# Optimization experiments

Hardware: AMD Instinct MI355X
Metric: run time of the kernel (lower is better)

Reference implementation:

```python
import jax, jax.numpy as jnp
import numpy as np

HIDDEN = 1024
HEADS = 12
HEAD_DIM = 64
NEG = -1e12


def _rope(x):
    # x: [B, N, H, d], rotate along seq axis (axis 1), interleaved pairs
    B, N, H, d = x.shape
    inv_freq = 1.0 / (10000.0 ** (jnp.arange(0, d, 2, dtype=jnp.float32) / d))  # [d/2]
    pos = jnp.arange(N, dtype=jnp.float32)
    ang = pos[:, None] * inv_freq[None, :]                 # [N, d/2]
    sin = jnp.repeat(jnp.sin(ang), 2, axis=-1)[None, :, None, :]  # [1,N,1,d]
    cos = jnp.repeat(jnp.cos(ang), 2, axis=-1)[None, :, None, :]
    even = x[..., ::2]
    odd = x[..., 1::2]
    rot = jnp.stack([-odd, even], axis=-1).reshape(B, N, H, d)
    return x * cos + rot * sin


def setup_inputs() -> dict:
    key = jax.random.key(0)
    k1, k2, k3, k4 = jax.random.split(key, 4)
    hidden_states = jax.random.normal(k1, (16, 512, HIDDEN), dtype=jnp.float32)
    attention_weights = jax.random.randint(k2, (16, 512), 0, 2, dtype=jnp.int32)
    W = jax.random.normal(k3, (HIDDEN, HEADS * HEAD_DIM * 2), dtype=jnp.float32) * 0.02
    b = jax.random.normal(k4, (HEADS * HEAD_DIM * 2,), dtype=jnp.float32) * 0.02
    return {"hidden_states": hidden_states, "attention_weights": attention_weights, "W": W, "b": b}


def reference(hidden_states, attention_weights, W, b):
    B, N, _ = hidden_states.shape
    proj = hidden_states @ W + b                            # [B,N,H*2*d]
    proj = proj.reshape(B, N, HEADS, 2, HEAD_DIM)
    q, k = proj[..., 0, :], proj[..., 1, :]                 # [B,N,H,d]
    q = _rope(q)
    k = _rope(k)
    q = q / (HEAD_DIM ** 0.5)
    scores = jnp.einsum('bnhd,bmhd->bhnm', q, k)            # [B,H,N,N]
    # mask padded keys (key dim only, matching the torch repeat pattern)
    key_mask = (attention_weights == 0)[:, None, None, :]   # [B,1,1,N]
    scores = jnp.where(key_mask, NEG, scores)
    # mask diagonal
    diag = jnp.eye(N, dtype=bool)[None, None, :, :]
    scores = jnp.where(diag, NEG, scores)
    return jax.nn.sigmoid(scores)
```

## Files before the change

### kernel.cpp

```cpp
#include <hip/hip_runtime.h>

#define HEADS 12
#define HIDDEN 1024
#define NOUT 1536
#define SEQ 512

typedef __bf16 bf16x8 __attribute__((ext_vector_type(8)));
typedef float f32x4 __attribute__((ext_vector_type(4)));

__device__ __forceinline__ void gload_lds16(const void* g, void* l) {
  __builtin_amdgcn_global_load_lds(
      (const __attribute__((address_space(1))) unsigned int*)g,
      (__attribute__((address_space(3))) unsigned int*)l, 16, 0, 0);
}

__device__ __forceinline__ unsigned short f2bf(float f) {
  union { float f; unsigned u; } x;
  x.f = f;
  unsigned r = x.u + 0x7fffu + ((x.u >> 16) & 1u);
  return (unsigned short)(r >> 16);
}

__global__ __launch_bounds__(256) void k_convert_hidden(const float* __restrict__ in,
                                                        unsigned short* __restrict__ out) {
  int i = blockIdx.x * 256 + threadIdx.x;
  float4 v = ((const float4*)in)[i];
  ushort4 o;
  o.x = f2bf(v.x); o.y = f2bf(v.y); o.z = f2bf(v.z); o.w = f2bf(v.w);
  ((ushort4*)out)[i] = o;
}

__global__ __launch_bounds__(256) void k_transpose_w(const float* __restrict__ W,
                                                     unsigned short* __restrict__ Wt) {
  __shared__ unsigned short t[32][33];
  int n0 = blockIdx.x * 32;
  int k0 = blockIdx.y * 32;
  int tx = threadIdx.x & 31;
  int ty = threadIdx.x >> 5;
#pragma unroll
  for (int i = 0; i < 4; ++i) {
    int k = k0 + ty + i * 8;
    t[ty + i * 8][tx] = f2bf(W[(size_t)k * NOUT + n0 + tx]);
  }
  __syncthreads();
#pragma unroll
  for (int i = 0; i < 4; ++i) {
    int n = n0 + ty + i * 8;
    Wt[(size_t)n * HIDDEN + k0 + tx] = t[tx][ty + i * 8];
  }
}

__global__ __launch_bounds__(256) void k_trig(float2* __restrict__ trig) {
  int i = blockIdx.x * 256 + threadIdx.x;
  int pos = i >> 5, j = i & 31;
  float inv = 1.0f / powf(10000.0f, (float)(2 * j) * (1.0f / 64.0f));
  float ang = (float)pos * inv;
  trig[i] = make_float2(cosf(ang), sinf(ang));
}

__global__ __launch_bounds__(256) void k_proj(const unsigned short* __restrict__ A,
                                              const unsigned short* __restrict__ Bt,
                                              const float* __restrict__ bias,
                                              const float2* __restrict__ trig,
                                              unsigned short* __restrict__ qb,
                                              unsigned short* __restrict__ kb) {
  __shared__ unsigned short As[128 * 64];
  __shared__ unsigned short Bs[128 * 64];
  const int h = blockIdx.x;
  const int m0 = blockIdx.y * 128;
  const int n0 = h * 128;
  const int tid = threadIdx.x;
  const int wave = tid >> 6, lane = tid & 63;
  const int l15 = lane & 15, l4 = lane >> 4;
  const int wr = wave >> 1, wc = wave & 1;

  f32x4 acc[4][4];
#pragma unroll
  for (int a = 0; a < 4; ++a)
#pragma unroll
    for (int b2 = 0; b2 < 4; ++b2) acc[a][b2] = (f32x4){0.f, 0.f, 0.f, 0.f};

  for (int kt = 0; kt < 16; ++kt) {
    __syncthreads();
    const int kbase = kt * 64;
#pragma unroll
    for (int i = 0; i < 4; ++i) {
      int chunk = i * 256 + tid;
      int r = chunk >> 3, c8 = chunk & 7;
      gload_lds16(A + (size_t)(m0 + r) * HIDDEN + kbase + c8 * 8, As + chunk * 8);
      gload_lds16(Bt + (size_t)(n0 + r) * HIDDEN + kbase + c8 * 8, Bs + chunk * 8);
    }
    asm volatile("s_waitcnt vmcnt(0)" ::: "memory");
    __syncthreads();
#pragma unroll
    for (int kk = 0; kk < 2; ++kk) {
      bf16x8 af[4], bv[4];
#pragma unroll
      for (int mi = 0; mi < 4; ++mi)
        af[mi] = *(const bf16x8*)(As + (wr * 64 + mi * 16 + l15) * 64 + kk * 32 + l4 * 8);
#pragma unroll
      for (int ni = 0; ni < 4; ++ni)
        bv[ni] = *(const bf16x8*)(Bs + (wc * 64 + ni * 16 + l15) * 64 + kk * 32 + l4 * 8);
#pragma unroll
      for (int mi = 0; mi < 4; ++mi)
#pragma unroll
        for (int ni = 0; ni < 4; ++ni)
          acc[mi][ni] = __builtin_amdgcn_mfma_f32_16x16x32_bf16(af[mi], bv[ni], acc[mi][ni], 0, 0, 0);
    }
  }

#pragma unroll
  for (int ni = 0; ni < 4; ++ni) {
    const int c = wc * 64 + ni * 16 + l15;
    const int qk = c >> 6;
    const int d = c & 63;
    const int j = d >> 1;
    const int odd = d & 1;
    const float bias_v = bias[n0 + c];
    unsigned short* dst = qk ? kb : qb;
    const float scale = qk ? 1.0f : 0.125f;
#pragma unroll
    for (int mi = 0; mi < 4; ++mi) {
#pragma unroll
      for (int jj = 0; jj < 4; ++jj) {
        const int row = wr * 64 + mi * 16 + l4 * 4 + jj;
        const int m = m0 + row;
        const int bb = m >> 9, pos = m & 511;
        float v = acc[mi][ni][jj] + bias_v;
        float p = __shfl_xor(v, 1);
        float2 cs = trig[pos * 32 + j];
        float o = odd ? (v * cs.x + p * cs.y) : (v * cs.x - p * cs.y);
        o *= scale;
        dst[(((size_t)bb * HEADS + h) * SEQ + pos) * 64 + d] = f2bf(o);
      }
    }
  }
}

__global__ __launch_bounds__(256) void k_scores(const unsigned short* __restrict__ qb,
                                                const unsigned short* __restrict__ kb,
                                                const int* __restrict__ aw,
                                                float* __restrict__ out) {
  __shared__ unsigned short Qs[128 * 64];
  __shared__ unsigned short Ks[128 * 64];
  const int bh = blockIdx.y;
  const int b = bh / HEADS;
  const int tq = blockIdx.x & 3, tk = blockIdx.x >> 2;
  const int q0 = tq * 128, k0 = tk * 128;
  const int tid = threadIdx.x;
  const int wave = tid >> 6, lane = tid & 63;
  const int l15 = lane & 15, l4 = lane >> 4;
  const int wr = wave >> 1, wc = wave & 1;

  const unsigned short* qsrc = qb + (size_t)bh * SEQ * 64;
  const unsigned short* ksrc = kb + (size_t)bh * SEQ * 64;

#pragma unroll
  for (int i = 0; i < 4; ++i) {
    int chunk = i * 256 + tid;
    int r = chunk >> 3, c8 = chunk & 7;
    gload_lds16(qsrc + (size_t)(q0 + r) * 64 + c8 * 8, Qs + chunk * 8);
    gload_lds16(ksrc + (size_t)(k0 + r) * 64 + c8 * 8, Ks + chunk * 8);
  }

  f32x4 acc[4][4];
#pragma unroll
  for (int a = 0; a < 4; ++a)
#pragma unroll
    for (int b2 = 0; b2 < 4; ++b2) acc[a][b2] = (f32x4){0.f, 0.f, 0.f, 0.f};

  asm volatile("s_waitcnt vmcnt(0)" ::: "memory");
  __syncthreads();

#pragma unroll
  for (int kk = 0; kk < 2; ++kk) {
    bf16x8 qf[4], kf[4];
#pragma unroll
    for (int mi = 0; mi < 4; ++mi)
      qf[mi] = *(const bf16x8*)(Qs + (wr * 64 + mi * 16 + l15) * 64 + kk * 32 + l4 * 8);
#pragma unroll
    for (int ni = 0; ni < 4; ++ni)
      kf[ni] = *(const bf16x8*)(Ks + (wc * 64 + ni * 16 + l15) * 64 + kk * 32 + l4 * 8);
#pragma unroll
    for (int mi = 0; mi < 4; ++mi)
#pragma unroll
      for (int ni = 0; ni < 4; ++ni)
        acc[mi][ni] = __builtin_amdgcn_mfma_f32_16x16x32_bf16(qf[mi], kf[ni], acc[mi][ni], 0, 0, 0);
  }

#pragma unroll
  for (int ni = 0; ni < 4; ++ni) {
    const int c = wc * 64 + ni * 16 + l15;
    const int key = k0 + c;
    const int awv = aw[b * SEQ + key];
#pragma unroll
    for (int mi = 0; mi < 4; ++mi) {
#pragma unroll
      for (int jj = 0; jj < 4; ++jj) {
        const int row = wr * 64 + mi * 16 + l4 * 4 + jj;
        const int nq = q0 + row;
        float s = acc[mi][ni][jj];
        float o = (awv == 0 || nq == key) ? 0.0f : 1.0f / (1.0f + __expf(-s));
        out[((size_t)bh * SEQ + nq) * SEQ + key] = o;
      }
    }
  }
}

extern "C" void kernel_launch(void* const* d_in, const int* in_sizes, int n_in,
                              void* d_out, int out_size, void* d_ws, size_t ws_size,
                              hipStream_t stream) {
  const float* hidden = (const float*)d_in[0];
  const int* aw = (const int*)d_in[1];
  const float* W = (const float*)d_in[2];
  const float* bias = (const float*)d_in[3];
  float* out = (float*)d_out;

  char* ws = (char*)d_ws;
  unsigned short* hidA = (unsigned short*)ws;
  unsigned short* Wt = (unsigned short*)(ws + 16777216);
  unsigned short* qb = (unsigned short*)(ws + 19922944);
  unsigned short* kb = (unsigned short*)(ws + 32505856);
  float2* trig = (float2*)(ws + 45088768);

  k_convert_hidden<<<8192, 256, 0, stream>>>(hidden, hidA);
  k_transpose_w<<<dim3(48, 32), 256, 0, stream>>>(W, Wt);
  k_trig<<<64, 256, 0, stream>>>(trig);
  k_proj<<<dim3(12, 64), 256, 0, stream>>>(hidA, Wt, bias, trig, qb, kb);
  k_scores<<<dim3(16, 192), 256, 0, stream>>>(qb, kb, aw, out);
}
```

Before: 131.0 us.

## Fuse prep kernels, swizzle block order for XCDs, loop key tiles in scores

Merges the hidden convert, weight transpose and trig table kernels into one launch, which removes two kernel launch gaps. It also remaps block indices with a stride-8 swizzle so neighbouring tiles land on the same XCD. The scores kernel now keeps one Q tile in LDS and loops over all four key tiles, reloading only K. This cuts the number of scores blocks from 3072 to 768, which reduces parallelism, and each K reload is serialized with barriers and no overlap.

```diff
diff --git a/kernel.cpp b/kernel.cpp
--- a/kernel.cpp
+++ b/kernel.cpp
@@ -21,41 +21,48 @@
   return (unsigned short)(r >> 16);
 }
 
-__global__ __launch_bounds__(256) void k_convert_hidden(const float* __restrict__ in,
-                                                        unsigned short* __restrict__ out) {
-  int i = blockIdx.x * 256 + threadIdx.x;
-  float4 v = ((const float4*)in)[i];
-  ushort4 o;
-  o.x = f2bf(v.x); o.y = f2bf(v.y); o.z = f2bf(v.z); o.w = f2bf(v.w);
-  ((ushort4*)out)[i] = o;
-}
-
-__global__ __launch_bounds__(256) void k_transpose_w(const float* __restrict__ W,
-                                                     unsigned short* __restrict__ Wt) {
+__device__ __forceinline__ int swz8(int b, int per) {
+  return (b & 7) * per + (b >> 3);
+}
+
+__global__ __launch_bounds__(256) void k_prep(const float* __restrict__ hidden,
+                                              unsigned short* __restrict__ hidA,
+                                              const float* __restrict__ W,
+                                              unsigned short* __restrict__ Wt,
+                                              float2* __restrict__ trig) {
   __shared__ unsigned short t[32][33];
-  int n0 = blockIdx.x * 32;
-  int k0 = blockIdx.y * 32;
-  int tx = threadIdx.x & 31;
-  int ty = threadIdx.x >> 5;
-#pragma unroll
-  for (int i = 0; i < 4; ++i) {
-    int k = k0 + ty + i * 8;
-    t[ty + i * 8][tx] = f2bf(W[(size_t)k * NOUT + n0 + tx]);
-  }
-  __syncthreads();
-#pragma unroll
-  for (int i = 0; i < 4; ++i) {
-    int n = n0 + ty + i * 8;
-    Wt[(size_t)n * HIDDEN + k0 + tx] = t[tx][ty + i * 8];
-  }
-}
-
-__global__ __launch_bounds__(256) void k_trig(float2* __restrict__ trig) {
-  int i = blockIdx.x * 256 + threadIdx.x;
-  int pos = i >> 5, j = i & 31;
-  float inv = 1.0f / powf(10000.0f, (float)(2 * j) * (1.0f / 64.0f));
-  float ang = (float)pos * inv;
-  trig[i] = make_float2(cosf(ang), sinf(ang));
+  const int bid = blockIdx.x;
+  const int tid = threadIdx.x;
+  if (bid < 8192) {
+    int i = bid * 256 + tid;
+    float4 v = ((const float4*)hidden)[i];
+    ushort4 o;
+    o.x = f2bf(v.x); o.y = f2bf(v.y); o.z = f2bf(v.z); o.w = f2bf(v.w);
+    ((ushort4*)hidA)[i] = o;
+  } else if (bid < 8192 + 1536) {
+    int tt = bid - 8192;
+    int n0 = (tt % 48) * 32;
+    int k0 = (tt / 48) * 32;
+    int tx = tid & 31;
+    int ty = tid >> 5;
+#pragma unroll
+    for (int i = 0; i < 4; ++i) {
+      int k = k0 + ty + i * 8;
+      t[ty + i * 8][tx] = f2bf(W[(size_t)k * NOUT + n0 + tx]);
+    }
+    __syncthreads();
+#pragma unroll
+    for (int i = 0; i < 4; ++i) {
+      int n = n0 + ty + i * 8;
+      Wt[(size_t)n * HIDDEN + k0 + tx] = t[tx][ty + i * 8];
+    }
+  } else {
+    int i = (bid - 9728) * 256 + tid;
+    int pos = i >> 5, j = i & 31;
+    float inv = 1.0f / powf(10000.0f, (float)(2 * j) * (1.0f / 64.0f));
+    float ang = (float)pos * inv;
+    trig[i] = make_float2(cosf(ang), sinf(ang));
+  }
 }
 
 __global__ __launch_bounds__(256) void k_proj(const unsigned short* __restrict__ A,
@@ -66,8 +73,9 @@
                                               unsigned short* __restrict__ kb) {
   __shared__ unsigned short As[128 * 64];
   __shared__ unsigned short Bs[128 * 64];
-  const int h = blockIdx.x;
-  const int m0 = blockIdx.y * 128;
+  const int lin = swz8(blockIdx.x, 96);
+  const int h = lin % 12;
+  const int m0 = (lin / 12) * 128;
   const int n0 = h * 128;
   const int tid = threadIdx.x;
   const int wave = tid >> 6, lane = tid & 63;
@@ -143,66 +151,80 @@
                                                 float* __restrict__ out) {
   __shared__ unsigned short Qs[128 * 64];
   __shared__ unsigned short Ks[128 * 64];
-  const int bh = blockIdx.y;
+  const int lin = swz8(blockIdx.x, 96);
+  const int bh = lin >> 2;
   const int b = bh / HEADS;
-  const int tq = blockIdx.x & 3, tk = blockIdx.x >> 2;
-  const int q0 = tq * 128, k0 = tk * 128;
+  const int q0 = (lin & 3) * 128;
   const int tid = threadIdx.x;
   const int wave = tid >> 6, lane = tid & 63;
   const int l15 = lane & 15, l4 = lane >> 4;
   const int wr = wave >> 1, wc = wave & 1;
 
-  const unsigned short* qsrc = qb + (size_t)bh * SEQ * 64;
+  const unsigned short* qsrc = qb + (size_t)bh * SEQ * 64 + (size_t)q0 * 64;
   const unsigned short* ksrc = kb + (size_t)bh * SEQ * 64;
 
 #pragma unroll
   for (int i = 0; i < 4; ++i) {
     int chunk = i * 256 + tid;
     int r = chunk >> 3, c8 = chunk & 7;
-    gload_lds16(qsrc + (size_t)(q0 + r) * 64 + c8 * 8, Qs + chunk * 8);
-    gload_lds16(ksrc + (size_t)(k0 + r) * 64 + c8 * 8, Ks + chunk * 8);
-  }
-
-  f32x4 acc[4][4];
-#pragma unroll
-  for (int a = 0; a < 4; ++a)
-#pragma unroll
-    for (int b2 = 0; b2 < 4; ++b2) acc[a][b2] = (f32x4){0.f, 0.f, 0.f, 0.f};
-
+    gload_lds16(qsrc + (size_t)r * 64 + c8 * 8, Qs + chunk * 8);
+    gload_lds16(ksrc + (size_t)r * 64 + c8 * 8, Ks + chunk * 8);
+  }
   asm volatile("s_waitcnt vmcnt(0)" ::: "memory");
   __syncthreads();
 
-#pragma unroll
-  for (int kk = 0; kk < 2; ++kk) {
-    bf16x8 qf[4], kf[4];
-#pragma unroll
-    for (int mi = 0; mi < 4; ++mi)
-      qf[mi] = *(const bf16x8*)(Qs + (wr * 64 + mi * 16 + l15) * 64 + kk * 32 + l4 * 8);
-#pragma unroll
-    for (int ni = 0; ni < 4; ++ni)
-      kf[ni] = *(const bf16x8*)(Ks + (wc * 64 + ni * 16 + l15) * 64 + kk * 32 + l4 * 8);
-#pragma unroll
-    for (int mi = 0; mi < 4; ++mi)
+  for (int tk = 0; tk < 4; ++tk) {
+    const int k0 = tk * 128;
+    f32x4 acc[4][4];
+#pragma unroll
+    for (int a = 0; a < 4; ++a)
+#pragma unroll
+      for (int b2 = 0; b2 < 4; ++b2) acc[a][b2] = (f32x4){0.f, 0.f, 0.f, 0.f};
+
+#pragma unroll
+    for (int kk = 0; kk < 2; ++kk) {
+      bf16x8 qf[4], kf[4];
+#pragma unroll
+      for (int mi = 0; mi < 4; ++mi)
+        qf[mi] = *(const bf16x8*)(Qs + (wr * 64 + mi * 16 + l15) * 64 + kk * 32 + l4 * 8);
 #pragma unroll
       for (int ni = 0; ni < 4; ++ni)
-        acc[mi][ni] = __builtin_amdgcn_mfma_f32_16x16x32_bf16(qf[mi], kf[ni], acc[mi][ni], 0, 0, 0);
-  }
-
-#pragma unroll
-  for (int ni = 0; ni < 4; ++ni) {
-    const int c = wc * 64 + ni * 16 + l15;
-    const int key = k0 + c;
-    const int awv = aw[b * SEQ + key];
-#pragma unroll
-    for (int mi = 0; mi < 4; ++mi) {
-#pragma unroll
-      for (int jj = 0; jj < 4; ++jj) {
-        const int row = wr * 64 + mi * 16 + l4 * 4 + jj;
-        const int nq = q0 + row;
-        float s = acc[mi][ni][jj];
-        float o = (awv == 0 || nq == key) ? 0.0f : 1.0f / (1.0f + __expf(-s));
-        out[((size_t)bh * SEQ + nq) * SEQ + key] = o;
+        kf[ni] = *(const bf16x8*)(Ks + (wc * 64 + ni * 16 + l15) * 64 + kk * 32 + l4 * 8);
+#pragma unroll
+      for (int mi = 0; mi < 4; ++mi)
+#pragma unroll
+        for (int ni = 0; ni < 4; ++ni)
+          acc[mi][ni] = __builtin_amdgcn_mfma_f32_16x16x32_bf16(qf[mi], kf[ni], acc[mi][ni], 0, 0, 0);
+    }
+
+#pragma unroll
+    for (int ni = 0; ni < 4; ++ni) {
+      const int c = wc * 64 + ni * 16 + l15;
+      const int key = k0 + c;
+      const int awv = aw[b * SEQ + key];
+#pragma unroll
+      for (int mi = 0; mi < 4; ++mi) {
+#pragma unroll
+        for (int jj = 0; jj < 4; ++jj) {
+          const int row = wr * 64 + mi * 16 + l4 * 4 + jj;
+          const int nq = q0 + row;
+          float s = acc[mi][ni][jj];
+          float o = (awv == 0 || nq == key) ? 0.0f : 1.0f / (1.0f + __expf(-s));
+          out[((size_t)bh * SEQ + nq) * SEQ + key] = o;
+        }
       }
+    }
+
+    if (tk < 3) {
+      __syncthreads();
+#pragma unroll
+      for (int i = 0; i < 4; ++i) {
+        int chunk = i * 256 + tid;
+        int r = chunk >> 3, c8 = chunk & 7;
+        gload_lds16(ksrc + (size_t)(k0 + 128 + r) * 64 + c8 * 8, Ks + chunk * 8);
+      }
+      asm volatile("s_waitcnt vmcnt(0)" ::: "memory");
+      __syncthreads();
     }
   }
 }
@@ -223,9 +245,7 @@
   unsigned short* kb = (unsigned short*)(ws + 32505856);
   float2* trig = (float2*)(ws + 45088768);
 
-  k_convert_hidden<<<8192, 256, 0, stream>>>(hidden, hidA);
-  k_transpose_w<<<dim3(48, 32), 256, 0, stream>>>(W, Wt);
-  k_trig<<<64, 256, 0, stream>>>(trig);
-  k_proj<<<dim3(12, 64), 256, 0, stream>>>(hidA, Wt, bias, trig, qb, kb);
-  k_scores<<<dim3(16, 192), 256, 0, stream>>>(qb, kb, aw, out);
-}
+  k_prep<<<9792, 256, 0, stream>>>(hidden, hidA, W, Wt, trig);
+  k_proj<<<768, 256, 0, stream>>>(hidA, Wt, bias, trig, qb, kb);
+  k_scores<<<768, 256, 0, stream>>>(qb, kb, aw, out);
+}
```

Result: faster. 124.7 us (-4.8%).
